# Kernel optimization log

Measured on AMD Instinct MI355X. Metric: run time of the kernel, lower is better.

## Reference

```python
import jax, jax.numpy as jnp
import numpy as np

# hyperparams matching init_kwargs
T_LEN = 1024
T_LATENCY = 7
TB = T_LATENCY + 1          # t_len_block
N_OUT = 1024
BATCH = 32
FS_SCALE = 10.0             # FastSigmoid default scale


@jax.custom_vjp
def fast_sigmoid(x):
    # forward: Heaviside; backward: fast-sigmoid surrogate
    return (x > 0).astype(x.dtype)

def _fs_fwd(x):
    return (x > 0).astype(x.dtype), x

def _fs_bwd(x, g):
    return (g / (FS_SCALE * jnp.abs(x) + 1.0) ** 2,)

fast_sigmoid.defvjp(_fs_fwd, _fs_bwd)


def setup_inputs() -> dict:
    key = jax.random.key(0)
    k1, k2, k3, k4 = jax.random.split(key, 4)
    x = jax.random.normal(k1, (T_LEN, BATCH, N_OUT), dtype=jnp.float32) * 0.6
    # raw params; forward applies the clamp/abs 'properties' of the module
    beta_raw = jax.random.uniform(k2, (N_OUT,), minval=0.7, maxval=0.99, dtype=jnp.float32)
    p_raw = jax.random.uniform(k3, (N_OUT,), minval=0.5, maxval=0.95, dtype=jnp.float32)
    b_raw = jax.random.uniform(k4, (N_OUT,), minval=0.2, maxval=1.0, dtype=jnp.float32)
    return {"x": x, "beta_raw": beta_raw, "p_raw": p_raw, "b_raw": b_raw}


def reference(x, beta_raw, p_raw, b_raw):
    T, B, N = x.shape
    tb = TB
    n_blocks = T // tb  # t_pad == 0 by construction
    dt = x.dtype

    # clamped properties
    beta = jnp.clip(beta_raw, 0.001, 0.999)          # [N]
    p = jnp.clip(jnp.abs(p_raw), 0.0, 0.999)         # [N]
    bb = jnp.clip(jnp.abs(b_raw), 0.001, 1.0)        # [N]

    t_idx = jnp.arange(tb)
    expo = t_idx[:, None] - t_idx[None, :]            # [tb,tb], t - s
    lower = expo >= 0
    # causal decay kernel: beta^(t-s) for s<=t  (grouped conv1d equivalent)
    beta_pow = jnp.where(lower[:, :, None],
                         beta[None, None, :] ** jnp.maximum(expo, 0)[:, :, None].astype(dt),
                         jnp.zeros((), dt))           # [tb,tb,N]
    # phi kernel: weight (t-s+1) for s<=t  (conv2d equivalent)
    phi = jnp.where(lower, (expo + 1).astype(dt), jnp.zeros((), dt))  # [tb,tb]
    p_exp = jnp.arange(1, tb + 1, dtype=dt)           # [tb]
    p_pow = p[None, :] ** p_exp[:, None]              # [tb,N]
    inv_p = 1.0 / p                                   # [N]

    def body(carry, x_slice):
        spikes, z, int_mem, a_kernel = carry          # [tb,B,N],[tb,B,N],[B,N],[tb,B,N]
        sg = jax.lax.stop_gradient(spikes)            # detach_spike_grad=True
        maskf = (jnp.max(sg, axis=0) > 0).astype(dt)  # [B,N] any spike in prev block
        # refractory masking of input
        xs = jnp.where(z < maskf[None], jnp.zeros((), dt), x_slice)
        v_init = int_mem * (1.0 - maskf)
        # adaptation update
        a_at_spike = jnp.sum(a_kernel * sg, axis=0) + inv_p          # [B,N]
        decay_steps = jnp.sum(z > 1, axis=0).astype(dt)              # [B,N]
        new_a = a_at_spike * jnp.power(p[None, :], decay_steps)
        a = a_kernel[-1] * (1.0 - maskf) + new_a * maskf             # [B,N]
        a_k = p_pow[:, None, :] * a[None]                             # [tb,B,N]
        v_th = 1.0 + bb[None, None, :] * a_k                          # [tb,B,N]
        # --- Block forward ---
        cur = xs.at[0].add(beta[None, :] * v_init)
        membrane = jnp.einsum('tsn,sbn->tbn', beta_pow, cur)          # causal decayed sum
        faulty = fast_sigmoid(membrane - v_th)                        # [tb,B,N] 0/1
        z_new = jnp.einsum('ts,sbn->tbn', phi, faulty)
        # g(): keep only entries exactly 1, straight-through grad
        spikes_new = z_new - jax.lax.stop_gradient(
            jnp.where(z_new == 1.0, jnp.zeros((), dt), z_new))
        return (spikes_new, z_new, membrane[-1], a_k), spikes_new

    z0 = jnp.zeros((tb, B, N), dt)
    carry0 = (z0, z0, jnp.zeros((B, N), dt), z0)
    xb = x.reshape(n_blocks, tb, B, N)
    _, out = jax.lax.scan(body, carry0, xb)
    return out.reshape(T, B, N)
```

## Files before the change

### kernel.cpp

```cpp
#include <hip/hip_runtime.h>


constexpr int T_LEN = 1024;
constexpr int TB    = 8;
constexpr int NBLK  = T_LEN / TB;
constexpr int BATCH = 32;
constexpr int NOUT  = 1024;
constexpr int BN    = BATCH * NOUT;
constexpr int PF    = 4;

__global__ __launch_bounds__(64, 1)
void snn_blocks_kernel(const float* __restrict__ x,
                       const float* __restrict__ beta_raw,
                       const float* __restrict__ p_raw,
                       const float* __restrict__ b_raw,
                       float* __restrict__ out)
{
    const int lane = threadIdx.x;
    const int gid  = blockIdx.x * 64 + lane;
    const int n    = gid & (NOUT - 1);

    double beta = (double)beta_raw[n];
    beta = beta < 0.001 ? 0.001 : (beta > 0.999 ? 0.999 : beta);
    double p = fabs((double)p_raw[n]);
    p = p > 0.999 ? 0.999 : p;
    double bb = fabs((double)b_raw[n]);
    bb = bb < 0.001 ? 0.001 : (bb > 1.0 ? 1.0 : bb);
    const double inv_p = 1.0 / p;

    double ppow[9];
    ppow[0] = 1.0;
#pragma unroll
    for (int i = 1; i <= 8; ++i) ppow[i] = ppow[i - 1] * p;

    double bbp[8];
#pragma unroll
    for (int t = 0; t < 8; ++t) bbp[t] = bb * ppow[t + 1];

    const double pp2 = ppow[2], pp4 = ppow[4], pp8 = ppow[8];

    double m = 0.0;
    double a = 0.0;
    int maskf  = 0;
    int firstp = 0;

    float fr[PF][8];
    const float* xb = x + gid;
    float* ob       = out + gid;

#pragma unroll
    for (int k = 0; k < PF; ++k)
#pragma unroll
        for (int t = 0; t < 8; ++t)
            fr[k][t] = xb[(ptrdiff_t)(k * TB + t) * BN];

#pragma unroll 1
    for (int r = 0; r < NBLK / PF; ++r) {
#pragma unroll
        for (int i = 0; i < PF; ++i) {
            const int blk = r * PF + i;

            double pf1 = p;
            pf1 *= (firstp & 1) ? p   : 1.0;
            pf1 *= (firstp & 2) ? pp2 : 1.0;
            pf1 *= (firstp & 4) ? pp4 : 1.0;
            const int dsteps = firstp ^ 7;
            double pd = (dsteps & 1) ? p : 1.0;
            pd *= (dsteps & 2) ? pp2 : 1.0;
            pd *= (dsteps & 4) ? pp4 : 1.0;
            const double new_a = (a * pf1 + inv_p) * pd;
            double vinit;
            if (maskf) { a = new_a;   vinit = 0.0; }
            else       { a = pp8 * a; vinit = m;   }

            const int zmask = maskf ? ((1 << firstp) - 1) : 0;

            int fbits = 0;
            double mm = vinit;
#pragma unroll
            for (int t = 0; t < 8; ++t) {
                const float xf = ((zmask >> t) & 1) ? 0.0f : fr[i][t];
                mm = beta * mm + (double)xf;
                const double vth = 1.0 + bbp[t] * a;
                fbits |= (mm - vth > 0.0) ? (1 << t) : 0;
            }
            m = mm;
            maskf  = (fbits != 0);
            firstp = fbits ? __builtin_ctz(fbits) : 0;

#pragma unroll
            for (int t = 0; t < 8; ++t) {
                const float sv = (maskf && t == firstp) ? 1.0f : 0.0f;
                __builtin_nontemporal_store(
                    sv, ob + (ptrdiff_t)(blk * TB + t) * BN);
            }

            const int pfb = blk + PF;
            if (pfb < NBLK) {
#pragma unroll
                for (int t = 0; t < 8; ++t)
                    fr[i][t] = xb[(ptrdiff_t)(pfb * TB + t) * BN];
            }
            __builtin_amdgcn_sched_barrier(0);
        }
    }
}

extern "C" void kernel_launch(void* const* d_in, const int* in_sizes, int n_in,
                              void* d_out, int out_size, void* d_ws, size_t ws_size,
                              hipStream_t stream) {
    const float* x        = (const float*)d_in[0];
    const float* beta_raw = (const float*)d_in[1];
    const float* p_raw    = (const float*)d_in[2];
    const float* b_raw    = (const float*)d_in[3];
    float* out            = (float*)d_out;

    dim3 grid(BN / 64);
    dim3 block(64);
    snn_blocks_kernel<<<grid, block, 0, stream>>>(x, beta_raw, p_raw, b_raw, out);
}
```

Measured before the change: 255.4 us.

## Vectorize global loads and stores through an LDS transpose and deepen prefetch

```diff
diff --git a/kernel.cpp b/kernel.cpp
--- a/kernel.cpp
+++ b/kernel.cpp
@@ -7,7 +7,9 @@
 constexpr int BATCH = 32;
 constexpr int NOUT  = 1024;
 constexpr int BN    = BATCH * NOUT;
-constexpr int PF    = 4;
+constexpr int PF    = 8;
+
+typedef float f4 __attribute__((ext_vector_type(4)));
 
 __global__ __launch_bounds__(64, 1)
 void snn_blocks_kernel(const float* __restrict__ x,
@@ -16,9 +18,16 @@
                        const float* __restrict__ b_raw,
                        float* __restrict__ out)
 {
+    __shared__ float inbuf[TB][64];
+    __shared__ float sbuf[TB][64];
+
     const int lane = threadIdx.x;
-    const int gid  = blockIdx.x * 64 + lane;
+    const int wg0  = blockIdx.x * 64;
+    const int gid  = wg0 + lane;
     const int n    = gid & (NOUT - 1);
+
+    const int rowoff = lane >> 4;
+    const int coloff = wg0 + (lane & 15) * 4;
 
     double beta = (double)beta_raw[n];
     beta = beta < 0.001 ? 0.001 : (beta > 0.999 ? 0.999 : beta);
@@ -44,21 +53,35 @@
     int maskf  = 0;
     int firstp = 0;
 
-    float fr[PF][8];
-    const float* xb = x + gid;
-    float* ob       = out + gid;
+    f4 fr[PF][2];
+
+    const float* xbase = x + (ptrdiff_t)rowoff * BN + coloff;
+    float* obase       = out + (ptrdiff_t)rowoff * BN + coloff;
 
 #pragma unroll
-    for (int k = 0; k < PF; ++k)
-#pragma unroll
-        for (int t = 0; t < 8; ++t)
-            fr[k][t] = xb[(ptrdiff_t)(k * TB + t) * BN];
+    for (int k = 0; k < PF; ++k) {
+        fr[k][0] = *(const f4*)(xbase + (ptrdiff_t)(k * TB) * BN);
+        fr[k][1] = *(const f4*)(xbase + (ptrdiff_t)(k * TB + 4) * BN);
+    }
 
 #pragma unroll 1
     for (int r = 0; r < NBLK / PF; ++r) {
 #pragma unroll
         for (int i = 0; i < PF; ++i) {
             const int blk = r * PF + i;
+
+            *(f4*)&inbuf[rowoff][(lane & 15) * 4]     = fr[i][0];
+            *(f4*)&inbuf[rowoff + 4][(lane & 15) * 4] = fr[i][1];
+
+            const int pfb = blk + PF;
+            if (pfb < NBLK) {
+                fr[i][0] = *(const f4*)(xbase + (ptrdiff_t)(pfb * TB) * BN);
+                fr[i][1] = *(const f4*)(xbase + (ptrdiff_t)(pfb * TB + 4) * BN);
+            }
+
+            float cur[8];
+#pragma unroll
+            for (int t = 0; t < 8; ++t) cur[t] = inbuf[t][lane];
 
             double pf1 = p;
             pf1 *= (firstp & 1) ? p   : 1.0;
@@ -79,7 +102,7 @@
             double mm = vinit;
 #pragma unroll
             for (int t = 0; t < 8; ++t) {
-                const float xf = ((zmask >> t) & 1) ? 0.0f : fr[i][t];
+                const float xf = ((zmask >> t) & 1) ? 0.0f : cur[t];
                 mm = beta * mm + (double)xf;
                 const double vth = 1.0 + bbp[t] * a;
                 fbits |= (mm - vth > 0.0) ? (1 << t) : 0;
@@ -89,18 +112,15 @@
             firstp = fbits ? __builtin_ctz(fbits) : 0;
 
 #pragma unroll
-            for (int t = 0; t < 8; ++t) {
-                const float sv = (maskf && t == firstp) ? 1.0f : 0.0f;
-                __builtin_nontemporal_store(
-                    sv, ob + (ptrdiff_t)(blk * TB + t) * BN);
-            }
+            for (int t = 0; t < 8; ++t)
+                sbuf[t][lane] = (maskf && t == firstp) ? 1.0f : 0.0f;
 
-            const int pfb = blk + PF;
-            if (pfb < NBLK) {
-#pragma unroll
-                for (int t = 0; t < 8; ++t)
-                    fr[i][t] = xb[(ptrdiff_t)(pfb * TB + t) * BN];
-            }
+            const float* sflat = &sbuf[0][0];
+            f4 s0 = *(const f4*)(sflat + lane * 4);
+            f4 s1 = *(const f4*)(sflat + 256 + lane * 4);
+            *(f4*)(obase + (ptrdiff_t)(blk * TB) * BN)     = s0;
+            *(f4*)(obase + (ptrdiff_t)(blk * TB + 4) * BN) = s1;
+
             __builtin_amdgcn_sched_barrier(0);
         }
     }
```

New measurement: 232.8 us. -8.8%, faster.

## Split time blocks across eight waves with LDS carry ring and async DMA loads

Applied to the files above, without the earlier changes.

```diff
diff --git a/kernel.cpp b/kernel.cpp
--- a/kernel.cpp
+++ b/kernel.cpp
@@ -7,17 +7,32 @@
 constexpr int BATCH = 32;
 constexpr int NOUT  = 1024;
 constexpr int BN    = BATCH * NOUT;
-constexpr int PF    = 4;
+constexpr int W     = 8;
+constexpr int NRND  = NBLK / W;
+constexpr int RING  = 16;
 
-__global__ __launch_bounds__(64, 1)
+__device__ __forceinline__ void dma16(const float* g, float* l) {
+    __builtin_amdgcn_global_load_lds(
+        (const __attribute__((address_space(1))) void*)g,
+        (__attribute__((address_space(3))) void*)l, 16, 0, 0);
+}
+
+__global__ __launch_bounds__(512, 4)
 void snn_blocks_kernel(const float* __restrict__ x,
                        const float* __restrict__ beta_raw,
                        const float* __restrict__ p_raw,
                        const float* __restrict__ b_raw,
                        float* __restrict__ out)
 {
-    const int lane = threadIdx.x;
-    const int gid  = blockIdx.x * 64 + lane;
+    __shared__ float    stg[W][2][TB * 64];
+    __shared__ double   carry_ma[RING][2 * 64];
+    __shared__ unsigned carry_pk[RING][64];
+
+    const int tid  = threadIdx.x;
+    const int lane = tid & 63;
+    const int w    = tid >> 6;
+    const int wg0  = blockIdx.x * 64;
+    const int gid  = wg0 + lane;
     const int n    = gid & (NOUT - 1);
 
     double beta = (double)beta_raw[n];
@@ -32,77 +47,109 @@
     ppow[0] = 1.0;
 #pragma unroll
     for (int i = 1; i <= 8; ++i) ppow[i] = ppow[i - 1] * p;
-
     double bbp[8];
 #pragma unroll
     for (int t = 0; t < 8; ++t) bbp[t] = bb * ppow[t + 1];
-
     const double pp2 = ppow[2], pp4 = ppow[4], pp8 = ppow[8];
 
-    double m = 0.0;
-    double a = 0.0;
-    int maskf  = 0;
-    int firstp = 0;
+    {
+        unsigned* pkflat = &carry_pk[0][0];
+        pkflat[tid]       = 0u;
+        pkflat[tid + 512] = 0u;
+    }
 
-    float fr[PF][8];
-    const float* xb = x + gid;
-    float* ob       = out + gid;
+    const float* xb_dma = x + (ptrdiff_t)(lane >> 4) * BN + wg0 + (lane & 15) * 4;
+    {
+        const float* g = xb_dma + (ptrdiff_t)(w * TB) * BN;
+        dma16(g,          &stg[w][0][0]);
+        dma16(g + 4 * BN, &stg[w][0][256]);
+    }
+    __syncthreads();
+
+    float* ob = out + gid;
+
+#pragma unroll 1
+    for (int r = 0; r < NRND; ++r) {
+        const int k = r * W + w;
+
+        if (r > 0)
+            asm volatile("s_waitcnt vmcnt(8)" ::: "memory");
+
+        float cur[8];
+#pragma unroll
+        for (int t = 0; t < 8; ++t)
+            cur[t] = stg[w][r & 1][t * 64 + lane];
+
+        double m, a;
+        int maskf, firstp;
+        if (k == 0) {
+            m = 0.0; a = 0.0; maskf = 0; firstp = 0;
+        } else {
+            const int slot = k & (RING - 1);
+            volatile unsigned* vpk = (volatile unsigned*)&carry_pk[slot][lane];
+            unsigned pk;
+            do { pk = *vpk; } while ((pk >> 8) != (unsigned)k);
+            asm volatile("" ::: "memory");
+            maskf  = (pk >> 4) & 1;
+            firstp = pk & 7;
+            m = carry_ma[slot][2 * lane];
+            a = carry_ma[slot][2 * lane + 1];
+        }
+
+        __builtin_amdgcn_s_setprio(1);
+
+        double pf1 = p;
+        pf1 *= (firstp & 1) ? p   : 1.0;
+        pf1 *= (firstp & 2) ? pp2 : 1.0;
+        pf1 *= (firstp & 4) ? pp4 : 1.0;
+        const int dsteps = firstp ^ 7;
+        double pd = (dsteps & 1) ? p : 1.0;
+        pd *= (dsteps & 2) ? pp2 : 1.0;
+        pd *= (dsteps & 4) ? pp4 : 1.0;
+        const double new_a = (a * pf1 + inv_p) * pd;
+        double vinit;
+        if (maskf) { a = new_a;   vinit = 0.0; }
+        else       { a = pp8 * a; vinit = m;   }
+
+        const int zmask = maskf ? ((1 << firstp) - 1) : 0;
+
+        int fbits = 0;
+        double mm = vinit;
+#pragma unroll
+        for (int t = 0; t < 8; ++t) {
+            const float xf = ((zmask >> t) & 1) ? 0.0f : cur[t];
+            mm = beta * mm + (double)xf;
+            const double vth = 1.0 + bbp[t] * a;
+            fbits |= (mm - vth > 0.0) ? (1 << t) : 0;
+        }
+        const int nmaskf  = (fbits != 0) ? 1 : 0;
+        const int nfirstp = fbits ? __builtin_ctz(fbits) : 0;
+
+        {
+            const int s2 = (k + 1) & (RING - 1);
+            carry_ma[s2][2 * lane]     = mm;
+            carry_ma[s2][2 * lane + 1] = a;
+            asm volatile("s_waitcnt lgkmcnt(0)" ::: "memory");
+            carry_pk[s2][lane] =
+                ((unsigned)(k + 1) << 8) | (nmaskf << 4) | nfirstp;
+        }
+        __builtin_amdgcn_s_setprio(0);
+        asm volatile("" ::: "memory");
+
+        if (k + W < NBLK) {
+            const float* g = xb_dma + (ptrdiff_t)((k + W) * TB) * BN;
+            float* l = &stg[w][(r + 1) & 1][0];
+            dma16(g,          l);
+            dma16(g + 4 * BN, l + 256);
+        }
+        asm volatile("" ::: "memory");
 
 #pragma unroll
-    for (int k = 0; k < PF; ++k)
-#pragma unroll
-        for (int t = 0; t < 8; ++t)
-            fr[k][t] = xb[(ptrdiff_t)(k * TB + t) * BN];
-
-#pragma unroll 1
-    for (int r = 0; r < NBLK / PF; ++r) {
-#pragma unroll
-        for (int i = 0; i < PF; ++i) {
-            const int blk = r * PF + i;
-
-            double pf1 = p;
-            pf1 *= (firstp & 1) ? p   : 1.0;
-            pf1 *= (firstp & 2) ? pp2 : 1.0;
-            pf1 *= (firstp & 4) ? pp4 : 1.0;
-            const int dsteps = firstp ^ 7;
-            double pd = (dsteps & 1) ? p : 1.0;
-            pd *= (dsteps & 2) ? pp2 : 1.0;
-            pd *= (dsteps & 4) ? pp4 : 1.0;
-            const double new_a = (a * pf1 + inv_p) * pd;
-            double vinit;
-            if (maskf) { a = new_a;   vinit = 0.0; }
-            else       { a = pp8 * a; vinit = m;   }
-
-            const int zmask = maskf ? ((1 << firstp) - 1) : 0;
-
-            int fbits = 0;
-            double mm = vinit;
-#pragma unroll
-            for (int t = 0; t < 8; ++t) {
-                const float xf = ((zmask >> t) & 1) ? 0.0f : fr[i][t];
-                mm = beta * mm + (double)xf;
-                const double vth = 1.0 + bbp[t] * a;
-                fbits |= (mm - vth > 0.0) ? (1 << t) : 0;
-            }
-            m = mm;
-            maskf  = (fbits != 0);
-            firstp = fbits ? __builtin_ctz(fbits) : 0;
-
-#pragma unroll
-            for (int t = 0; t < 8; ++t) {
-                const float sv = (maskf && t == firstp) ? 1.0f : 0.0f;
-                __builtin_nontemporal_store(
-                    sv, ob + (ptrdiff_t)(blk * TB + t) * BN);
-            }
-
-            const int pfb = blk + PF;
-            if (pfb < NBLK) {
-#pragma unroll
-                for (int t = 0; t < 8; ++t)
-                    fr[i][t] = xb[(ptrdiff_t)(pfb * TB + t) * BN];
-            }
-            __builtin_amdgcn_sched_barrier(0);
+        for (int t = 0; t < 8; ++t) {
+            const float sv = (nmaskf && t == nfirstp) ? 1.0f : 0.0f;
+            ob[(ptrdiff_t)(k * TB + t) * BN] = sv;
         }
+        asm volatile("" ::: "memory");
     }
 }
 
@@ -116,6 +163,6 @@
     float* out            = (float*)d_out;
 
     dim3 grid(BN / 64);
-    dim3 block(64);
+    dim3 block(512);
     snn_blocks_kernel<<<grid, block, 0, stream>>>(x, beta_raw, p_raw, b_raw, out);
 }
```

Measured after the change: 237.7 us. -6.9%, faster.
